# Optimization experiments

Hardware: AMD Instinct MI355X
Metric: run time of the kernel (lower is better)

## Reference

```python
import jax, jax.numpy as jnp
import numpy as np

N = 500_000
D = 256
G = 1024


def setup_inputs() -> dict:
    key = jax.random.key(0)
    k1, k2, k3, k4, k5, k6 = jax.random.split(key, 6)
    x = jax.random.normal(k1, (N, D), dtype=jnp.float32)
    batch = jnp.sort(jax.random.randint(k2, (N,), 0, G).astype(jnp.int64))
    s = 1.0 / np.sqrt(D)
    W1 = jax.random.normal(k3, (D, D), dtype=jnp.float32) * s
    b1 = jax.random.normal(k4, (D,), dtype=jnp.float32) * 0.01
    W2 = jax.random.normal(k5, (D, 1), dtype=jnp.float32) * s
    b2 = jax.random.normal(k6, (1,), dtype=jnp.float32) * 0.01
    return {"x": x, "batch": batch, "num_graphs": G,
            "W1": W1, "b1": b1, "W2": W2, "b2": b2}


def reference(x, batch, num_graphs, W1, b1, W2, b2):
    # gate MLP: Linear -> Tanh -> Linear  => [N, 1]
    h = jnp.tanh(x @ W1 + b1)
    scores = (h @ W2 + b2)[:, 0]  # [N]
    # segment softmax over nodes grouped by graph id
    seg_max = jax.ops.segment_max(scores, batch, num_segments=num_graphs)  # [G]
    # empty segments give -inf max, but no node indexes them
    e = jnp.exp(scores - seg_max[batch])  # [N]
    denom = jax.ops.segment_sum(e, batch, num_segments=num_graphs)  # [G]
    attn = e / denom[batch]  # [N]
    weighted = x * attn[:, None]  # [N, D]
    # global_add_pool: scatter-add nodes into graphs
    return jax.ops.segment_sum(weighted, batch, num_segments=num_graphs)  # [G, D]
```

## Files before the change

### kernel.cpp

```cpp
#include <hip/hip_runtime.h>
#include <hip/hip_bf16.h>

#define D 256

typedef __attribute__((ext_vector_type(8))) short bf16x8;
typedef __attribute__((ext_vector_type(4))) float f32x4;

__device__ __forceinline__ unsigned short f2bf(float a) {
    unsigned int u = __float_as_uint(a);
    u = (u + 0x7fffu + ((u >> 16) & 1u)) >> 16;
    return (unsigned short)u;
}

__device__ __forceinline__ unsigned int cvt_pk_bf16(float a, float b) {
    unsigned int r;
    asm("v_cvt_pk_bf16_f32 %0, %1, %2" : "=v"(r) : "v"(a), "v"(b));
    return r;
}

__device__ __forceinline__ float fast_tanh(float v) {
    float a = __builtin_fabsf(v);
    float e = __builtin_amdgcn_exp2f(a * -2.88539008177793f);
    float t = (1.0f - e) * __builtin_amdgcn_rcpf(1.0f + e);
    return __builtin_copysignf(t, v);
}

__global__ void pack_w1_k(const float* __restrict__ W1, unsigned short* __restrict__ W1p) {
    int p = blockIdx.x * 256 + threadIdx.x;
    int e  = p & 7;
    int l  = (p >> 3) & 63;
    int cb = (p >> 9) & 15;
    int kk = p >> 13;
    int k   = 32 * kk + 8 * (l >> 4) + e;
    int col = 16 * cb + (l & 15);
    W1p[p] = f2bf(W1[k * D + col]);
}

__global__ void zero_k(float* __restrict__ p, int n) {
    int i = blockIdx.x * 256 + threadIdx.x;
    if (i < n) p[i] = 0.f;
}

__global__ void __launch_bounds__(256, 2)
fused_k(const float* __restrict__ x,
        const unsigned short* __restrict__ W1p,
        const float* __restrict__ b1,
        const float* __restrict__ W2,
        const float* __restrict__ b2,
        const int* __restrict__ batch, int N,
        float* __restrict__ accb, float* __restrict__ den) {
    __shared__ __align__(16) unsigned int Xl[64 * 128];
    __shared__ float scpart[4][64];
    __shared__ float red[4][256];
    __shared__ float erow[64];
    __shared__ int   bids[64];

    const int tid = threadIdx.x;
    const int w   = tid >> 6;
    const int l   = tid & 63;
    const int l15 = l & 15;
    const int g4  = l >> 4;
    const int row0 = blockIdx.x * 64;

    float4 xv[16];
    const float4* x4 = reinterpret_cast<const float4*>(x);
    if (row0 + 64 <= N) {
        #pragma unroll
        for (int it = 0; it < 16; ++it) {
            int r = 4 * it + w;
            float4 v = x4[(size_t)(row0 + r) * 64 + l];
            xv[it] = v;
            unsigned int lo = cvt_pk_bf16(v.x, v.y);
            unsigned int hi = cvt_pk_bf16(v.z, v.w);
            int uidx = r * 128 + ((l * 2) ^ ((r & 7) << 2));
            *reinterpret_cast<uint2*>(&Xl[uidx]) = make_uint2(lo, hi);
        }
    } else {
        #pragma unroll
        for (int it = 0; it < 16; ++it) {
            int r = 4 * it + w;
            float4 v = make_float4(0.f, 0.f, 0.f, 0.f);
            if (row0 + r < N) v = x4[(size_t)(row0 + r) * 64 + l];
            xv[it] = v;
            unsigned int lo = cvt_pk_bf16(v.x, v.y);
            unsigned int hi = cvt_pk_bf16(v.z, v.w);
            int uidx = r * 128 + ((l * 2) ^ ((r & 7) << 2));
            *reinterpret_cast<uint2*>(&Xl[uidx]) = make_uint2(lo, hi);
        }
    }
    if (tid < 64) bids[tid] = batch[min(row0 + tid, N - 1)];
    __syncthreads();

    f32x4 acc[4][4];
    #pragma unroll
    for (int m = 0; m < 4; ++m)
        #pragma unroll
        for (int n = 0; n < 4; ++n)
            acc[m][n] = (f32x4){0.f, 0.f, 0.f, 0.f};

    #pragma unroll
    for (int kk = 0; kk < 8; ++kk) {
        bf16x8 bfr[4];
        #pragma unroll
        for (int n = 0; n < 4; ++n) {
            const bf16x8* bp = reinterpret_cast<const bf16x8*>(
                W1p + (size_t)(((kk * 16) + (w * 4 + n)) * 64 + l) * 8);
            bfr[n] = *bp;
        }
        bf16x8 afr[4];
        #pragma unroll
        for (int m = 0; m < 4; ++m) {
            int r = 16 * m + l15;
            int cbyte = 64 * kk + 16 * g4;
            int uidx = r * 128 + (((cbyte >> 2)) ^ ((r & 7) << 2));
            afr[m] = *reinterpret_cast<const bf16x8*>(&Xl[uidx]);
        }
        #pragma unroll
        for (int m = 0; m < 4; ++m)
            #pragma unroll
            for (int n = 0; n < 4; ++n)
                acc[m][n] = __builtin_amdgcn_mfma_f32_16x16x32_bf16(afr[m], bfr[n], acc[m][n], 0, 0, 0);
    }

    float part[4][4];
    #pragma unroll
    for (int m = 0; m < 4; ++m)
        #pragma unroll
        for (int r = 0; r < 4; ++r) part[m][r] = 0.f;

    #pragma unroll
    for (int n = 0; n < 4; ++n) {
        int col = 64 * w + 16 * n + l15;
        float b1v = b1[col];
        float w2v = W2[col];
        #pragma unroll
        for (int m = 0; m < 4; ++m)
            #pragma unroll
            for (int r = 0; r < 4; ++r) {
                float h = fast_tanh(acc[m][n][r] + b1v);
                part[m][r] += h * w2v;
            }
    }

    #pragma unroll
    for (int m = 0; m < 4; ++m)
        #pragma unroll
        for (int r = 0; r < 4; ++r) {
            float p = part[m][r];
            p += __shfl_xor(p, 8, 16);
            p += __shfl_xor(p, 4, 16);
            p += __shfl_xor(p, 2, 16);
            p += __shfl_xor(p, 1, 16);
            if (l15 == 0) scpart[w][16 * m + 4 * g4 + r] = p;
        }
    __syncthreads();

    if (tid < 64) {
        float s = scpart[0][tid] + scpart[1][tid] + scpart[2][tid] + scpart[3][tid] + b2[0];
        erow[tid] = (row0 + tid < N)
                  ? __builtin_amdgcn_exp2f(s * 1.4426950408889634f)
                  : 0.f;
    }
    __syncthreads();

    const int g0 = bids[0], g1 = bids[63];
    for (int g = g0; g <= g1; ++g) {
        float4 a = make_float4(0.f, 0.f, 0.f, 0.f);
        #pragma unroll
        for (int it = 0; it < 16; ++it) {
            int r = 4 * it + w;
            float e = (bids[r] == g) ? erow[r] : 0.f;
            a.x += e * xv[it].x;
            a.y += e * xv[it].y;
            a.z += e * xv[it].z;
            a.w += e * xv[it].w;
        }
        red[w][l * 4 + 0] = a.x;
        red[w][l * 4 + 1] = a.y;
        red[w][l * 4 + 2] = a.z;
        red[w][l * 4 + 3] = a.w;
        __syncthreads();
        float s = red[0][tid] + red[1][tid] + red[2][tid] + red[3][tid];
        atomicAdd(&accb[(size_t)g * D + tid], s);
        if (w == 0) {
            float e = (bids[l] == g) ? erow[l] : 0.f;
            e += __shfl_xor(e, 32);
            e += __shfl_xor(e, 16);
            e += __shfl_xor(e, 8);
            e += __shfl_xor(e, 4);
            e += __shfl_xor(e, 2);
            e += __shfl_xor(e, 1);
            if (l == 0) atomicAdd(&den[g], e);
        }
        __syncthreads();
    }
}

__global__ void __launch_bounds__(256)
norm_k(const float* __restrict__ accb, const float* __restrict__ den,
       float* __restrict__ out) {
    int g = blockIdx.x;
    float dv = den[g];
    float inv = (dv > 0.f) ? 1.0f / dv : 0.f;
    out[(size_t)g * D + threadIdx.x] = accb[(size_t)g * D + threadIdx.x] * inv;
}

extern "C" void kernel_launch(void* const* d_in, const int* in_sizes, int n_in,
                              void* d_out, int out_size, void* d_ws, size_t ws_size,
                              hipStream_t stream) {
    const float* x     = (const float*)d_in[0];
    const int*   batch = (const int*)d_in[1];
    const float* W1    = (const float*)d_in[3];
    const float* b1    = (const float*)d_in[4];
    const float* W2    = (const float*)d_in[5];
    const float* b2    = (const float*)d_in[6];
    float* out = (float*)d_out;

    const int N = in_sizes[0] / D;
    const int G = out_size / D;

    char* ws = (char*)d_ws;
    unsigned short* W1p = (unsigned short*)ws;
    float* accb = (float*)(ws + 131072);
    float* den  = (float*)(ws + 131072 + (size_t)G * D * 4);

    zero_k<<<dim3((G * D + G + 255) / 256), dim3(256), 0, stream>>>(accb, G * D + G);
    pack_w1_k<<<dim3(256), dim3(256), 0, stream>>>(W1, W1p);
    fused_k<<<dim3((N + 63) / 64), dim3(256), 0, stream>>>(x, W1p, b1, W2, b2, batch, N, accb, den);
    norm_k<<<dim3(G), dim3(256), 0, stream>>>(accb, den, out);
}
```

Measured before the change: 210.6 us.

## Halve rows per block, stage fp32 x in LDS, raise occupancy

Each block now handles 32 rows instead of 64 and keeps x in shared memory as fp32 with a swizzled layout, instead of holding it in registers as float4s and storing a bf16 copy. The A fragments are converted to bf16 on the fly when read from LDS, and the pooling step re-reads fp32 x from LDS. This frees registers so the launch bound can target 4 blocks per CU, aiming to hide the latency of the memory-bound x stream. The cost is twice as many blocks, so every block reloads W1 and issues more segment atomics, and there is extra LDS traffic and conversion work per block.

```diff
diff --git a/kernel.cpp b/kernel.cpp
--- a/kernel.cpp
+++ b/kernel.cpp
@@ -23,6 +23,10 @@
     float e = __builtin_amdgcn_exp2f(a * -2.88539008177793f);
     float t = (1.0f - e) * __builtin_amdgcn_rcpf(1.0f + e);
     return __builtin_copysignf(t, v);
+}
+
+__device__ __forceinline__ int xf_off(int c, int r, int q) {
+    return ((c << 10) + (r << 5) + (q << 4)) ^ ((c & 3) << 5) ^ ((r & 4) << 2);
 }
 
 __global__ void pack_w1_k(const float* __restrict__ W1, unsigned short* __restrict__ W1p) {
@@ -41,7 +45,7 @@
     if (i < n) p[i] = 0.f;
 }
 
-__global__ void __launch_bounds__(256, 2)
+__global__ void __launch_bounds__(256, 4)
 fused_k(const float* __restrict__ x,
         const unsigned short* __restrict__ W1p,
         const float* __restrict__ b1,
@@ -49,51 +53,38 @@
         const float* __restrict__ b2,
         const int* __restrict__ batch, int N,
         float* __restrict__ accb, float* __restrict__ den) {
-    __shared__ __align__(16) unsigned int Xl[64 * 128];
-    __shared__ float scpart[4][64];
+    __shared__ __align__(16) float Xf[8192];
     __shared__ float red[4][256];
-    __shared__ float erow[64];
-    __shared__ int   bids[64];
+    __shared__ float scpart[4][32];
+    __shared__ float erow[32];
+    __shared__ int   bids[32];
 
     const int tid = threadIdx.x;
     const int w   = tid >> 6;
     const int l   = tid & 63;
     const int l15 = l & 15;
     const int g4  = l >> 4;
-    const int row0 = blockIdx.x * 64;
-
-    float4 xv[16];
+    const int row0 = blockIdx.x * 32;
+
+    char* xb = reinterpret_cast<char*>(Xf);
+
     const float4* x4 = reinterpret_cast<const float4*>(x);
-    if (row0 + 64 <= N) {
-        #pragma unroll
-        for (int it = 0; it < 16; ++it) {
-            int r = 4 * it + w;
-            float4 v = x4[(size_t)(row0 + r) * 64 + l];
-            xv[it] = v;
-            unsigned int lo = cvt_pk_bf16(v.x, v.y);
-            unsigned int hi = cvt_pk_bf16(v.z, v.w);
-            int uidx = r * 128 + ((l * 2) ^ ((r & 7) << 2));
-            *reinterpret_cast<uint2*>(&Xl[uidx]) = make_uint2(lo, hi);
-        }
-    } else {
-        #pragma unroll
-        for (int it = 0; it < 16; ++it) {
-            int r = 4 * it + w;
-            float4 v = make_float4(0.f, 0.f, 0.f, 0.f);
-            if (row0 + r < N) v = x4[(size_t)(row0 + r) * 64 + l];
-            xv[it] = v;
-            unsigned int lo = cvt_pk_bf16(v.x, v.y);
-            unsigned int hi = cvt_pk_bf16(v.z, v.w);
-            int uidx = r * 128 + ((l * 2) ^ ((r & 7) << 2));
-            *reinterpret_cast<uint2*>(&Xl[uidx]) = make_uint2(lo, hi);
-        }
-    }
-    if (tid < 64) bids[tid] = batch[min(row0 + tid, N - 1)];
+    const bool full = (row0 + 32 <= N);
+    #pragma unroll
+    for (int it = 0; it < 8; ++it) {
+        int idx = it * 256 + tid;
+        int r    = idx >> 6;
+        int col4 = idx & 63;
+        float4 v = make_float4(0.f, 0.f, 0.f, 0.f);
+        if (full || row0 + r < N) v = x4[(size_t)(row0 + r) * 64 + col4];
+        *reinterpret_cast<float4*>(xb + xf_off(col4 >> 1, r, col4 & 1)) = v;
+    }
+    if (tid < 32) bids[tid] = batch[min(row0 + tid, N - 1)];
     __syncthreads();
 
-    f32x4 acc[4][4];
-    #pragma unroll
-    for (int m = 0; m < 4; ++m)
+    f32x4 acc[2][4];
+    #pragma unroll
+    for (int m = 0; m < 2; ++m)
         #pragma unroll
         for (int n = 0; n < 4; ++n)
             acc[m][n] = (f32x4){0.f, 0.f, 0.f, 0.f};
@@ -107,24 +98,31 @@
                 W1p + (size_t)(((kk * 16) + (w * 4 + n)) * 64 + l) * 8);
             bfr[n] = *bp;
         }
-        bf16x8 afr[4];
-        #pragma unroll
-        for (int m = 0; m < 4; ++m) {
+        bf16x8 afr[2];
+        #pragma unroll
+        for (int m = 0; m < 2; ++m) {
             int r = 16 * m + l15;
-            int cbyte = 64 * kk + 16 * g4;
-            int uidx = r * 128 + (((cbyte >> 2)) ^ ((r & 7) << 2));
-            afr[m] = *reinterpret_cast<const bf16x8*>(&Xl[uidx]);
-        }
-        #pragma unroll
-        for (int m = 0; m < 4; ++m)
+            int c = 4 * kk + g4;
+            int o0 = xf_off(c, r, 0);
+            float4 f0 = *reinterpret_cast<const float4*>(xb + o0);
+            float4 f1 = *reinterpret_cast<const float4*>(xb + (o0 ^ 16));
+            uint4 u;
+            u.x = cvt_pk_bf16(f0.x, f0.y);
+            u.y = cvt_pk_bf16(f0.z, f0.w);
+            u.z = cvt_pk_bf16(f1.x, f1.y);
+            u.w = cvt_pk_bf16(f1.z, f1.w);
+            afr[m] = *reinterpret_cast<bf16x8*>(&u);
+        }
+        #pragma unroll
+        for (int m = 0; m < 2; ++m)
             #pragma unroll
             for (int n = 0; n < 4; ++n)
                 acc[m][n] = __builtin_amdgcn_mfma_f32_16x16x32_bf16(afr[m], bfr[n], acc[m][n], 0, 0, 0);
     }
 
-    float part[4][4];
-    #pragma unroll
-    for (int m = 0; m < 4; ++m)
+    float part[2][4];
+    #pragma unroll
+    for (int m = 0; m < 2; ++m)
         #pragma unroll
         for (int r = 0; r < 4; ++r) part[m][r] = 0.f;
 
@@ -134,7 +132,7 @@
         float b1v = b1[col];
         float w2v = W2[col];
         #pragma unroll
-        for (int m = 0; m < 4; ++m)
+        for (int m = 0; m < 2; ++m)
             #pragma unroll
             for (int r = 0; r < 4; ++r) {
                 float h = fast_tanh(acc[m][n][r] + b1v);
@@ -143,7 +141,7 @@
     }
 
     #pragma unroll
-    for (int m = 0; m < 4; ++m)
+    for (int m = 0; m < 2; ++m)
         #pragma unroll
         for (int r = 0; r < 4; ++r) {
             float p = part[m][r];
@@ -155,7 +153,7 @@
         }
     __syncthreads();
 
-    if (tid < 64) {
+    if (tid < 32) {
         float s = scpart[0][tid] + scpart[1][tid] + scpart[2][tid] + scpart[3][tid] + b2[0];
         erow[tid] = (row0 + tid < N)
                   ? __builtin_amdgcn_exp2f(s * 1.4426950408889634f)
@@ -163,17 +161,20 @@
     }
     __syncthreads();
 
-    const int g0 = bids[0], g1 = bids[63];
+    const int g0 = bids[0], g1 = bids[31];
+    const int pc = l >> 1;
+    const int pq = l & 1;
     for (int g = g0; g <= g1; ++g) {
         float4 a = make_float4(0.f, 0.f, 0.f, 0.f);
         #pragma unroll
-        for (int it = 0; it < 16; ++it) {
+        for (int it = 0; it < 8; ++it) {
             int r = 4 * it + w;
             float e = (bids[r] == g) ? erow[r] : 0.f;
-            a.x += e * xv[it].x;
-            a.y += e * xv[it].y;
-            a.z += e * xv[it].z;
-            a.w += e * xv[it].w;
+            float4 v = *reinterpret_cast<const float4*>(xb + xf_off(pc, r, pq));
+            a.x += e * v.x;
+            a.y += e * v.y;
+            a.z += e * v.z;
+            a.w += e * v.w;
         }
         red[w][l * 4 + 0] = a.x;
         red[w][l * 4 + 1] = a.y;
@@ -183,7 +184,8 @@
         float s = red[0][tid] + red[1][tid] + red[2][tid] + red[3][tid];
         atomicAdd(&accb[(size_t)g * D + tid], s);
         if (w == 0) {
-            float e = (bids[l] == g) ? erow[l] : 0.f;
+            float e = 0.f;
+            if (l < 32) e = (bids[l] == g) ? erow[l] : 0.f;
             e += __shfl_xor(e, 32);
             e += __shfl_xor(e, 16);
             e += __shfl_xor(e, 8);
@@ -226,6 +228,6 @@
 
     zero_k<<<dim3((G * D + G + 255) / 256), dim3(256), 0, stream>>>(accb, G * D + G);
     pack_w1_k<<<dim3(256), dim3(256), 0, stream>>>(W1, W1p);
-    fused_k<<<dim3((N + 63) / 64), dim3(256), 0, stream>>>(x, W1p, b1, W2, b2, batch, N, accb, den);
+    fused_k<<<dim3((N + 31) / 32), dim3(256), 0, stream>>>(x, W1p, b1, W2, b2, batch, N, accb, den);
     norm_k<<<dim3(G), dim3(256), 0, stream>>>(accb, den, out);
 }
```

Result: slower. 226.7 us (+7.6%).
